# Performance work log

Hardware: AMD Instinct MI355X
Metric: run time of the kernel (lower is better)

The kernel has to match this reference:

```python
import jax, jax.numpy as jnp
import numpy as np

# Static config (from set_param of the wrapped deformable conv)
N, CIN, H, W = 8, 64, 128, 128
COUT, KH, KW = 64, 3, 3
STRIDE, PAD, DIL = 1, 1, 1
WEIGHT_BIT = 8
K = KH * KW
HO = (H + 2 * PAD - DIL * (KH - 1) - 1) // STRIDE + 1
WO = (W + 2 * PAD - DIL * (KW - 1) - 1) // STRIDE + 1


def setup_inputs() -> dict:
    key = jax.random.key(0)
    k1, k2, k3 = jax.random.split(key, 3)
    x = jax.random.normal(k1, (N, CIN, H, W), dtype=jnp.float32)
    offset = jax.random.normal(k2, (N, 2 * K, HO, WO), dtype=jnp.float32)
    weight = jax.random.normal(k3, (COUT, CIN, KH, KW), dtype=jnp.float32) * 0.05
    return {"x": x, "offset": offset, "weight": weight}


def quantize_weight_symmetric(w, bits):
    # HAWQ/CoDeNet symmetric per-tensor quant: scale = max(|min|,|max|)/n,
    # q = clamp(round(w/scale), -n-1, n) * scale, straight-through estimator.
    n = 2 ** (bits - 1) - 1
    sat = jnp.maximum(jnp.abs(w.min()), jnp.abs(w.max()))
    scale = jnp.maximum(sat, 1e-8) / n
    wq = jnp.clip(jnp.round(w / scale), -n - 1, n) * scale
    return w + jax.lax.stop_gradient(wq - w)


def deform_conv2d(x, offset, weight):
    # x: [N,C,H,W]; offset: [N, 2*K, HO, WO] (y,x interleaved per kernel tap)
    # Base sampling grid for each kernel tap and output location.
    ky, kx = jnp.meshgrid(jnp.arange(KH), jnp.arange(KW), indexing='ij')
    ky = ky.reshape(K).astype(jnp.float32)  # [K]
    kx = kx.reshape(K).astype(jnp.float32)
    ho = jnp.arange(HO, dtype=jnp.float32)
    wo = jnp.arange(WO, dtype=jnp.float32)
    base_y = ho[None, :, None] * STRIDE - PAD + ky[:, None, None] * DIL  # [K,HO,1]
    base_x = wo[None, None, :] * STRIDE - PAD + kx[:, None, None] * DIL  # [K,1,WO]

    off = offset.reshape(N, K, 2, HO, WO)
    py = base_y[None] + off[:, :, 0]  # [N,K,HO,WO]
    px = base_x[None] + off[:, :, 1]

    y0 = jnp.floor(py)
    x0 = jnp.floor(px)
    dy = py - y0
    dx = px - x0
    y0i = y0.astype(jnp.int32)
    x0i = x0.astype(jnp.int32)

    xf = x.reshape(N, CIN, H * W)

    def gather_corner(yi, xi, wgt):
        # zero padding outside the image
        valid = (yi >= 0) & (yi < H) & (xi >= 0) & (xi < W)
        idx = jnp.clip(yi, 0, H - 1) * W + jnp.clip(xi, 0, W - 1)  # [N,K,HO,WO]
        vals = jax.vmap(lambda xn, idn: xn[:, idn.reshape(-1)])(xf, idx)
        vals = vals.reshape(N, CIN, K, HO, WO)
        return vals * (wgt * valid.astype(wgt.dtype))[:, None]  # [N,1,K,HO,WO]

    sampled = (
        gather_corner(y0i, x0i, (1.0 - dy) * (1.0 - dx))
        + gather_corner(y0i, x0i + 1, (1.0 - dy) * dx)
        + gather_corner(y0i + 1, x0i, dy * (1.0 - dx))
        + gather_corner(y0i + 1, x0i + 1, dy * dx)
    )  # [N,CIN,K,HO,WO]

    out = jnp.einsum('nckhw,ock->nohw', sampled, weight.reshape(COUT, CIN, K))
    return out


def reference(x, offset, weight):
    wq = quantize_weight_symmetric(weight, WEIGHT_BIT)
    return deform_conv2d(x, offset, wq)
```

## Files before the change

kernel.cpp:

```cpp
#include <hip/hip_runtime.h>
#include <hip/hip_bf16.h>

#define NB    8
#define CCH   64
#define HH    128
#define WW    128
#define KTAP  9
#define HW    (HH * WW)
#define KSTEPS 18
#define NW    36864

typedef _Float16 f16x8 __attribute__((ext_vector_type(8)));
typedef _Float16 f16x2 __attribute__((ext_vector_type(2)));
typedef __attribute__((ext_vector_type(4))) float f32x4;

__device__ inline unsigned int pack_f16(float a, float b) {
    f16x2 h;
    h[0] = (_Float16)a;
    h[1] = (_Float16)b;
    return __builtin_bit_cast(unsigned int, h);
}

__device__ inline f16x8 as_f16x8(uint4 u) { return __builtin_bit_cast(f16x8, u); }

__global__ __launch_bounds__(256) void prep_kernel(const float* __restrict__ x,
                                                   const float* __restrict__ w,
                                                   unsigned int* __restrict__ xt32,
                                                   uint4* __restrict__ bq) {
    __shared__ float tile[64 * 65];
    const int t = threadIdx.x;
    const int bid = blockIdx.x;

    if (bid < 2048) {
        const int n = bid >> 8;
        const int pbase = (bid & 255) * 64;
        #pragma unroll
        for (int i = 0; i < 4; i++) {
            int idx = i * 256 + t;
            int c = idx >> 4, f4 = idx & 15;
            float4 v = *(const float4*)&x[((size_t)(n * CCH + c)) * HW + pbase + f4 * 4];
            float* d = &tile[c * 65 + f4 * 4];
            d[0] = v.x; d[1] = v.y; d[2] = v.z; d[3] = v.w;
        }
        __syncthreads();
        const int px = t >> 2, c4 = t & 3;
        float f[16];
        #pragma unroll
        for (int j = 0; j < 16; j++) f[j] = tile[(c4 * 16 + j) * 65 + px];
        unsigned int o8[8];
        #pragma unroll
        for (int i = 0; i < 8; i++) o8[i] = pack_f16(f[2 * i], f[2 * i + 1]);
        uint4* dst = (uint4*)&xt32[((size_t)(n * HW + pbase + px)) * 32 + c4 * 8];
        dst[0] = make_uint4(o8[0], o8[1], o8[2], o8[3]);
        dst[1] = make_uint4(o8[4], o8[5], o8[6], o8[7]);
    } else {
        float m0 = 0.f, m1 = 0.f, m2 = 0.f, m3 = 0.f;
        for (int i = t; i < NW; i += 1024) {
            m0 = fmaxf(m0, fabsf(w[i]));
            m1 = fmaxf(m1, fabsf(w[i + 256]));
            m2 = fmaxf(m2, fabsf(w[i + 512]));
            m3 = fmaxf(m3, fabsf(w[i + 768]));
        }
        float m = fmaxf(fmaxf(m0, m1), fmaxf(m2, m3));
        #pragma unroll
        for (int off = 32; off > 0; off >>= 1)
            m = fmaxf(m, __shfl_down(m, off));
        if ((t & 63) == 0) tile[t >> 6] = m;
        __syncthreads();
        m = fmaxf(fmaxf(tile[0], tile[1]), fmaxf(tile[2], tile[3]));
        const float scale = fmaxf(m, 1e-8f) / 127.f;
        const float inv_scale = 1.f / scale;

        const int rec = (bid - 2048) * 256 + t;
        int nt  = rec / (KSTEPS * 64);
        int rem = rec - nt * (KSTEPS * 64);
        int s    = rem >> 6;
        int lane = rem & 63;
        int quad = lane >> 4, n16 = lane & 15;
        int o = nt * 16 + n16;
        unsigned int u[4];
        #pragma unroll
        for (int jj = 0; jj < 4; jj++) {
            float q[2];
            #pragma unroll
            for (int h = 0; h < 2; h++) {
                int k   = s * 32 + quad * 8 + 2 * jj + h;
                int c   = k & 63;
                int tap = k >> 6;
                float v  = w[(o * CCH + c) * KTAP + tap];
                float qq = rintf(v * inv_scale);
                q[h] = fminf(fmaxf(qq, -128.f), 127.f) * scale;
            }
            u[jj] = pack_f16(q[0], q[1]);
        }
        bq[rec] = make_uint4(u[0], u[1], u[2], u[3]);
    }
}

__global__ __launch_bounds__(256) void deform_mfma(const unsigned short* __restrict__ xt,
                                                   const float* __restrict__ offset,
                                                   const uint4* __restrict__ bq,
                                                   float* __restrict__ out) {
    __shared__ _Float16 Abuf[2][2][4096];
    __shared__ unsigned int SC[576];
    __shared__ uint2 SW[576];

    const int t    = threadIdx.x;
    const int wid  = t >> 6;
    const int lane = t & 63;
    const int quad = lane >> 4, n16 = lane & 15;
    const int bid  = blockIdx.x;
    const int n    = bid & 7;
    const int px0  = (bid >> 3) * 64;
    const int pl   = t >> 2;
    const int c4   = t & 3;
    const int cb   = c4 * 16;
    const int p7   = pl & 7;

    const char* xb = (const char*)(xt + (size_t)n * HW * CCH);
    const float* offn = offset + (size_t)n * 2 * KTAP * HW;

    for (int u = t; u < 576; u += 256) {
        const int tap = u >> 6, p = u & 63;
        const int ppx = px0 + p;
        const int ho = ppx >> 7, wo = ppx & 127;
        const int ky = tap / 3, kx = tap - 3 * ky;
        const float py  = (float)(ho - 1 + ky) + offn[(2 * tap) * HW + ppx];
        const float pxf = (float)(wo - 1 + kx) + offn[(2 * tap + 1) * HW + ppx];
        const float fy = floorf(py), fx = floorf(pxf);
        const int y0 = (int)fy, x0 = (int)fx;
        const float dy = py - fy, dx = pxf - fx;
        const int y1 = y0 + 1, x1 = x0 + 1;
        const bool vy0 = (y0 >= 0) && (y0 < HH);
        const bool vy1 = (y1 >= 0) && (y1 < HH);
        const bool vx0 = (x0 >= 0) && (x0 < WW);
        const bool vx1 = (x1 >= 0) && (x1 < WW);
        const int y0c = min(max(y0, 0), HH - 1);
        const int y1c = min(max(y1, 0), HH - 1);
        const int x0c = min(max(x0, 0), WW - 1);
        const int x1c = min(max(x1, 0), WW - 1);
        const float w00 = (1.f - dy) * (1.f - dx) * ((vy0 && vx0) ? 1.f : 0.f);
        const float w01 = (1.f - dy) * dx         * ((vy0 && vx1) ? 1.f : 0.f);
        const float w10 = dy * (1.f - dx)         * ((vy1 && vx0) ? 1.f : 0.f);
        const float w11 = dy * dx                 * ((vy1 && vx1) ? 1.f : 0.f);
        SC[u] = (unsigned)(y0c | (x0c << 7) | (y1c << 14) | (x1c << 21));
        SW[u] = make_uint2(pack_f16(w00, w01), pack_f16(w10, w11));
    }
    __syncthreads();

    f32x4 acc[4];
    #pragma unroll
    for (int mt = 0; mt < 4; mt++) acc[mt] = (f32x4){0.f, 0.f, 0.f, 0.f};

    uint4 rset[16];
    uint4 bset[2][4];

    auto gather8 = [&](int tap, uint4* r) {
        const unsigned int cc = SC[tap * 64 + pl];
        const int y0b = (int)(cc & 127) << 14;
        const int x0b = (int)((cc >> 7) & 127) << 7;
        const int y1b = (int)((cc >> 14) & 127) << 14;
        const int x1b = (int)(cc >> 21) << 7;
        const char* q00 = xb + (y0b | x0b) + cb;
        const char* q01 = xb + (y0b | x1b) + cb;
        const char* q10 = xb + (y1b | x0b) + cb;
        const char* q11 = xb + (y1b | x1b) + cb;
        r[0] = *(const uint4*)q00; r[1] = *(const uint4*)(q00 + 64);
        r[2] = *(const uint4*)q01; r[3] = *(const uint4*)(q01 + 64);
        r[4] = *(const uint4*)q10; r[5] = *(const uint4*)(q10 + 64);
        r[6] = *(const uint4*)q11; r[7] = *(const uint4*)(q11 + 64);
    };
    auto issue_stage = [&](int s) {
        gather8(2 * s, rset);
        if (s < 4) gather8(2 * s + 1, rset + 8);
        const int nk = (s < 4) ? 4 : 2;
        for (int k = 0; k < nk; k++)
            bset[s & 1][k] = bq[((size_t)wid * KSTEPS + 4 * s + k) * 64 + lane];
    };
    auto blend1 = [&](int tap, const uint4* r, _Float16* sub) {
        const uint2 ww = SW[tap * 64 + pl];
        const f16x2 wA = __builtin_bit_cast(f16x2, ww.x);
        const f16x2 wB = __builtin_bit_cast(f16x2, ww.y);
        f16x8 sa = as_f16x8(r[0]) * wA[0];
        sa += as_f16x8(r[2]) * wA[1];
        sa += as_f16x8(r[4]) * wB[0];
        sa += as_f16x8(r[6]) * wB[1];
        f16x8 sb = as_f16x8(r[1]) * wA[0];
        sb += as_f16x8(r[3]) * wA[1];
        sb += as_f16x8(r[5]) * wB[0];
        sb += as_f16x8(r[7]) * wB[1];
        *(f16x8*)&sub[pl * 64 + ((c4 ^ p7) * 8)]       = sa;
        *(f16x8*)&sub[pl * 64 + (((4 + c4) ^ p7) * 8)] = sb;
    };
    auto blend_stage = [&](int s) {
        blend1(2 * s, rset, Abuf[s & 1][0]);
        if (s < 4) blend1(2 * s + 1, rset + 8, Abuf[s & 1][1]);
    };
    auto mma_stage = [&](int s) {
        const int nk = (s < 4) ? 4 : 2;
        for (int ks = 0; ks < nk; ks++) {
            const _Float16* sub = Abuf[s & 1][ks >> 1];
            const f16x8 bf = __builtin_bit_cast(f16x8, bset[s & 1][ks]);
            #pragma unroll
            for (int mt = 0; mt < 4; mt++) {
                const int rr = mt * 16 + n16;
                const int slot = ((ks & 1) * 4 + quad) ^ (n16 & 7);
                const f16x8 a = *(const f16x8*)&sub[rr * 64 + slot * 8];
                acc[mt] = __builtin_amdgcn_mfma_f32_16x16x32_f16(a, bf, acc[mt], 0, 0, 0);
            }
        }
    };

    issue_stage(0);
    #pragma unroll
    for (int s = 0; s < 5; s++) {
        blend_stage(s);
        if (s < 4) issue_stage(s + 1);
        __syncthreads();
        mma_stage(s);
    }

    const int o = wid * 16 + n16;
    #pragma unroll
    for (int mt = 0; mt < 4; mt++) {
        float4 v = make_float4(acc[mt].x, acc[mt].y, acc[mt].z, acc[mt].w);
        float* dst = out + ((size_t)(n * CCH + o)) * HW + px0 + mt * 16 + quad * 4;
        *(float4*)dst = v;
    }
}

extern "C" void kernel_launch(void* const* d_in, const int* in_sizes, int n_in,
                              void* d_out, int out_size, void* d_ws, size_t ws_size,
                              hipStream_t stream) {
    const float* x      = (const float*)d_in[0];
    const float* offset = (const float*)d_in[1];
    const float* weight = (const float*)d_in[2];
    float* out = (float*)d_out;

    unsigned char* ws = (unsigned char*)d_ws;
    uint4*        bq   = (uint4*)ws;
    unsigned int* xt32 = (unsigned int*)(ws + 131072);
    const unsigned short* xt = (const unsigned short*)xt32;

    prep_kernel<<<2048 + 18, 256, 0, stream>>>(x, weight, xt32, bq);
    deform_mfma<<<2048, 256, 0, stream>>>(xt, offset, bq, out);
}
```

Before: 133.9 us.

## Pipeline one tap per stage with 8 threads per pixel gathering 16B each

Restructures the gather/blend/MFMA pipeline to handle one kernel tap per stage (9 stages) instead of two taps per stage (5 stages). Each thread now covers two pixels with 16-byte channel slices, so one pixel's 128-byte row is read by 8 adjacent threads. This halves the register gather set and the LDS A buffer, which may raise occupancy and coalescing. The cost is more barrier synchronizations and less in-flight memory per stage.

```diff
diff --git a/kernel.cpp b/kernel.cpp
--- a/kernel.cpp
+++ b/kernel.cpp
@@ -101,7 +101,7 @@
                                                    const float* __restrict__ offset,
                                                    const uint4* __restrict__ bq,
                                                    float* __restrict__ out) {
-    __shared__ _Float16 Abuf[2][2][4096];
+    __shared__ __align__(16) _Float16 Abuf[2][4096];
     __shared__ unsigned int SC[576];
     __shared__ uint2 SW[576];
 
@@ -112,10 +112,8 @@
     const int bid  = blockIdx.x;
     const int n    = bid & 7;
     const int px0  = (bid >> 3) * 64;
-    const int pl   = t >> 2;
-    const int c4   = t & 3;
-    const int cb   = c4 * 16;
-    const int p7   = pl & 7;
+    const int pg   = t >> 3;
+    const int q8   = t & 7;
 
     const char* xb = (const char*)(xt + (size_t)n * HW * CCH);
     const float* offn = offset + (size_t)n * 2 * KTAP * HW;
@@ -152,59 +150,51 @@
     #pragma unroll
     for (int mt = 0; mt < 4; mt++) acc[mt] = (f32x4){0.f, 0.f, 0.f, 0.f};
 
-    uint4 rset[16];
-    uint4 bset[2][4];
-
-    auto gather8 = [&](int tap, uint4* r) {
-        const unsigned int cc = SC[tap * 64 + pl];
-        const int y0b = (int)(cc & 127) << 14;
-        const int x0b = (int)((cc >> 7) & 127) << 7;
-        const int y1b = (int)((cc >> 14) & 127) << 14;
-        const int x1b = (int)(cc >> 21) << 7;
-        const char* q00 = xb + (y0b | x0b) + cb;
-        const char* q01 = xb + (y0b | x1b) + cb;
-        const char* q10 = xb + (y1b | x0b) + cb;
-        const char* q11 = xb + (y1b | x1b) + cb;
-        r[0] = *(const uint4*)q00; r[1] = *(const uint4*)(q00 + 64);
-        r[2] = *(const uint4*)q01; r[3] = *(const uint4*)(q01 + 64);
-        r[4] = *(const uint4*)q10; r[5] = *(const uint4*)(q10 + 64);
-        r[6] = *(const uint4*)q11; r[7] = *(const uint4*)(q11 + 64);
-    };
+    uint4 rset[8];
+    uint4 bset[2][2];
+
     auto issue_stage = [&](int s) {
-        gather8(2 * s, rset);
-        if (s < 4) gather8(2 * s + 1, rset + 8);
-        const int nk = (s < 4) ? 4 : 2;
-        for (int k = 0; k < nk; k++)
-            bset[s & 1][k] = bq[((size_t)wid * KSTEPS + 4 * s + k) * 64 + lane];
-    };
-    auto blend1 = [&](int tap, const uint4* r, _Float16* sub) {
-        const uint2 ww = SW[tap * 64 + pl];
-        const f16x2 wA = __builtin_bit_cast(f16x2, ww.x);
-        const f16x2 wB = __builtin_bit_cast(f16x2, ww.y);
-        f16x8 sa = as_f16x8(r[0]) * wA[0];
-        sa += as_f16x8(r[2]) * wA[1];
-        sa += as_f16x8(r[4]) * wB[0];
-        sa += as_f16x8(r[6]) * wB[1];
-        f16x8 sb = as_f16x8(r[1]) * wA[0];
-        sb += as_f16x8(r[3]) * wA[1];
-        sb += as_f16x8(r[5]) * wB[0];
-        sb += as_f16x8(r[7]) * wB[1];
-        *(f16x8*)&sub[pl * 64 + ((c4 ^ p7) * 8)]       = sa;
-        *(f16x8*)&sub[pl * 64 + (((4 + c4) ^ p7) * 8)] = sb;
+        #pragma unroll
+        for (int r = 0; r < 2; r++) {
+            const int p = pg + 32 * r;
+            const unsigned int cc = SC[s * 64 + p];
+            const int y0b = (int)(cc & 127) << 14;
+            const int x0b = (int)((cc >> 7) & 127) << 7;
+            const int y1b = (int)((cc >> 14) & 127) << 14;
+            const int x1b = (int)(cc >> 21) << 7;
+            const char* base = xb + q8 * 16;
+            rset[4 * r + 0] = *(const uint4*)(base + (y0b | x0b));
+            rset[4 * r + 1] = *(const uint4*)(base + (y0b | x1b));
+            rset[4 * r + 2] = *(const uint4*)(base + (y1b | x0b));
+            rset[4 * r + 3] = *(const uint4*)(base + (y1b | x1b));
+        }
+        bset[s & 1][0] = bq[((size_t)wid * KSTEPS + 2 * s) * 64 + lane];
+        bset[s & 1][1] = bq[((size_t)wid * KSTEPS + 2 * s + 1) * 64 + lane];
     };
     auto blend_stage = [&](int s) {
-        blend1(2 * s, rset, Abuf[s & 1][0]);
-        if (s < 4) blend1(2 * s + 1, rset + 8, Abuf[s & 1][1]);
+        _Float16* dst = Abuf[s & 1];
+        #pragma unroll
+        for (int r = 0; r < 2; r++) {
+            const int p = pg + 32 * r;
+            const uint2 ww = SW[s * 64 + p];
+            const f16x2 wA = __builtin_bit_cast(f16x2, ww.x);
+            const f16x2 wB = __builtin_bit_cast(f16x2, ww.y);
+            f16x8 sa = as_f16x8(rset[4 * r + 0]) * wA[0];
+            sa += as_f16x8(rset[4 * r + 1]) * wA[1];
+            sa += as_f16x8(rset[4 * r + 2]) * wB[0];
+            sa += as_f16x8(rset[4 * r + 3]) * wB[1];
+            *(f16x8*)&dst[p * 64 + ((q8 ^ (p & 7)) * 8)] = sa;
+        }
     };
     auto mma_stage = [&](int s) {
-        const int nk = (s < 4) ? 4 : 2;
-        for (int ks = 0; ks < nk; ks++) {
-            const _Float16* sub = Abuf[s & 1][ks >> 1];
+        const _Float16* sub = Abuf[s & 1];
+        #pragma unroll
+        for (int ks = 0; ks < 2; ks++) {
             const f16x8 bf = __builtin_bit_cast(f16x8, bset[s & 1][ks]);
+            const int slot = (ks * 4 + quad) ^ (n16 & 7);
             #pragma unroll
             for (int mt = 0; mt < 4; mt++) {
                 const int rr = mt * 16 + n16;
-                const int slot = ((ks & 1) * 4 + quad) ^ (n16 & 7);
                 const f16x8 a = *(const f16x8*)&sub[rr * 64 + slot * 8];
                 acc[mt] = __builtin_amdgcn_mfma_f32_16x16x32_f16(a, bf, acc[mt], 0, 0, 0);
             }
@@ -213,9 +203,9 @@
 
     issue_stage(0);
     #pragma unroll
-    for (int s = 0; s < 5; s++) {
+    for (int s = 0; s < 9; s++) {
         blend_stage(s);
-        if (s < 4) issue_stage(s + 1);
+        if (s < 8) issue_stage(s + 1);
         __syncthreads();
         mma_stage(s);
     }
```

New measurement: 127.1 us. 1.05x faster.
